# Kernel optimization log

Hardware: AMD Instinct MI355X
Metric: run time of the kernel (lower is better)

## Reference

```python
import jax, jax.numpy as jnp
import numpy as np

N = 100000   # nodes
D = 128      # in_feats
H = 128      # hidden_size
E = 500000   # message edges
EP = 100000  # positive pair edges
EN = 500000  # negative pair edges


def setup_inputs() -> dict:
    key = jax.random.key(0)
    ks = jax.random.split(key, 20)
    s = 1.0 / np.sqrt(H)
    f32 = jnp.float32
    inp = {
        "x": jax.random.normal(ks[0], (N, D), f32),
        "src": jax.random.randint(ks[1], (E,), 0, N, jnp.int32),
        "dst": jax.random.randint(ks[2], (E,), 0, N, jnp.int32),
        "pos_src": jax.random.randint(ks[3], (EP,), 0, N, jnp.int32),
        "pos_dst": jax.random.randint(ks[4], (EP,), 0, N, jnp.int32),
        "neg_src": jax.random.randint(ks[5], (EN,), 0, N, jnp.int32),
        "neg_dst": jax.random.randint(ks[6], (EN,), 0, N, jnp.int32),
        # SAGEConv layer 0 (in->hid) and layer 1 (hid->hid)
        "W_self0": jax.random.normal(ks[7], (D, H), f32) * s,
        "W_neigh0": jax.random.normal(ks[8], (D, H), f32) * s,
        "b0": jnp.zeros((H,), f32),
        "W_self1": jax.random.normal(ks[9], (H, H), f32) * s,
        "W_neigh1": jax.random.normal(ks[10], (H, H), f32) * s,
        "b1": jnp.zeros((H,), f32),
        # EdgeDecoder MLP: hid->hid->hid->1
        "dW1": jax.random.normal(ks[11], (H, H), f32) * s,
        "db1": jnp.zeros((H,), f32),
        "dW2": jax.random.normal(ks[12], (H, H), f32) * s,
        "db2": jnp.zeros((H,), f32),
        "dW3": jax.random.normal(ks[13], (H, 1), f32) * s,
        "db3": jnp.zeros((1,), f32),
    }
    return inp


def _sage_mean(h, src, dst, W_self, W_neigh, b, n_nodes):
    # mean-aggregate neighbor features: gather src feats, segment-sum over dst
    agg = jax.ops.segment_sum(h[src], dst, num_segments=n_nodes)       # [N, d]
    deg = jax.ops.segment_sum(jnp.ones((src.shape[0],), h.dtype), dst,
                              num_segments=n_nodes)                     # [N]
    h_neigh = agg / jnp.maximum(deg, 1.0)[:, None]
    return h @ W_self + h_neigh @ W_neigh + b


def _edge_decode(h, e_src, e_dst, W1, b1, W2, b2, W3, b3):
    z = h[e_src] * h[e_dst]                    # [E_pair, H]
    z = jax.nn.relu(z @ W1 + b1)
    z = jax.nn.relu(z @ W2 + b2)
    return z @ W3 + b3                         # [E_pair, 1]


def reference(x, src, dst, pos_src, pos_dst, neg_src, neg_dst,
              W_self0, W_neigh0, b0, W_self1, W_neigh1, b1,
              dW1, db1, dW2, db2, dW3, db3):
    n = x.shape[0]
    h = jax.nn.relu(_sage_mean(x, src, dst, W_self0, W_neigh0, b0, n))
    h = _sage_mean(h, src, dst, W_self1, W_neigh1, b1, n)  # no act on last layer
    h_pos = _edge_decode(h, pos_src, pos_dst, dW1, db1, dW2, db2, dW3, db3)
    h_neg = _edge_decode(h, neg_src, neg_dst, dW1, db1, dW2, db2, dW3, db3)
    return (h_pos, h_neg)
```

## Files before the change

kernel.cpp:

```cpp
#include <hip/hip_runtime.h>
#include <hip/hip_bf16.h>

#define HD 128

typedef unsigned int u32;
typedef unsigned short u16;
typedef __attribute__((ext_vector_type(8))) short short8;
typedef __attribute__((ext_vector_type(4))) float f32x4;

__device__ __forceinline__ float bf2f(u16 u) {
    return __uint_as_float(((u32)u) << 16);
}
__device__ __forceinline__ u16 f2bf(float f) {
    u32 u = __float_as_uint(f);
    u32 r = (u + 0x7fffu + ((u >> 16) & 1u)) >> 16;
    return (u16)r;
}
__device__ __forceinline__ u32 pk2bf(float lo, float hi) {
    __hip_bfloat162 h = __float22bfloat162_rn(make_float2(lo, hi));
    union { __hip_bfloat162 h; u32 u; } cv; cv.h = h;
    return cv.u;
}
__device__ __forceinline__ u32 hmul2(u32 a, u32 b) {
    union { u32 u; __hip_bfloat162 h; } x, y, r;
    x.u = a; y.u = b;
    r.h = __hmul2(x.h, y.h);
    return r.u;
}
__device__ __forceinline__ float ldf(const void* p, size_t i, bool f32m) {
    return f32m ? ((const float*)p)[i] : bf2f(((const u16*)p)[i]);
}
__device__ __forceinline__ int swz(int row, int col) {
    return row * 128 + ((((col >> 3) ^ (row & 7)) << 3) | (col & 7));
}
__device__ __forceinline__ void acc8_bf16(uint4 v, float* a) {
    a[0] += __uint_as_float(v.x << 16); a[1] += __uint_as_float(v.x & 0xffff0000u);
    a[2] += __uint_as_float(v.y << 16); a[3] += __uint_as_float(v.y & 0xffff0000u);
    a[4] += __uint_as_float(v.z << 16); a[5] += __uint_as_float(v.z & 0xffff0000u);
    a[6] += __uint_as_float(v.w << 16); a[7] += __uint_as_float(v.w & 0xffff0000u);
}

__global__ void detect_mode(const u32* __restrict__ x, int* __restrict__ mode) {
    __shared__ int cnt_s;
    if (threadIdx.x == 0) cnt_s = 0;
    __syncthreads();
    u32 e = (x[threadIdx.x] >> 23) & 0xFFu;
    if (e >= 90u && e < 170u) atomicAdd(&cnt_s, 1);
    __syncthreads();
    if (threadIdx.x == 0) mode[0] = (cnt_s >= 128) ? 1 : 0;
}

__global__ void cast_x(const void* __restrict__ x, u16* __restrict__ xb,
                       const int* __restrict__ gmode, int total8) {
    const bool f32m = gmode[0] != 0;
    int i = blockIdx.x * 256 + threadIdx.x;
    int stride = gridDim.x * 256;
    if (f32m) {
        for (; i < total8; i += stride) {
            const float* p = (const float*)x + (size_t)i * 8;
            float4 v0 = *(const float4*)p, v1 = *(const float4*)(p + 4);
            uint4 o;
            o.x = pk2bf(v0.x, v0.y); o.y = pk2bf(v0.z, v0.w);
            o.z = pk2bf(v1.x, v1.y); o.w = pk2bf(v1.z, v1.w);
            *(uint4*)(xb + (size_t)i * 8) = o;
        }
    } else {
        for (; i < total8; i += stride) {
            *(uint4*)(xb + (size_t)i * 8) =
                *(const uint4*)((const u16*)x + (size_t)i * 8);
        }
    }
}

__global__ void pack_w6(const void* __restrict__ W0, const void* __restrict__ W1,
                        const void* __restrict__ W2, const void* __restrict__ W3,
                        const void* __restrict__ W4, const void* __restrict__ W5,
                        u16* __restrict__ out, const int* __restrict__ gmode) {
    const bool f32m = gmode[0] != 0;
    int gid = blockIdx.x * 256 + threadIdx.x;
    if (gid >= 6 * 16384) return;
    int sel = gid >> 14, idx = gid & 16383;
    const void* W = sel == 0 ? W0 : sel == 1 ? W1 : sel == 2 ? W2 :
                    sel == 3 ? W3 : sel == 4 ? W4 : W5;
    int j = idx & 7, lane = (idx >> 3) & 63, ks = (idx >> 9) & 3, nt = idx >> 11;
    int k = ks * 32 + (lane >> 4) * 8 + j;
    int n = nt * 16 + (lane & 15);
    out[gid] = f2bf(ldf(W, (size_t)k * HD + n, f32m));
}

__global__ void cnt_count(const int* __restrict__ dst, int* __restrict__ cnt, int e) {
    int i = blockIdx.x * 256 + threadIdx.x;
    if (i < e) atomicAdd(&cnt[dst[i]], 1);
}

__global__ void scan_blocks(const int* __restrict__ cnt, int* __restrict__ rowptr,
                            int* __restrict__ bsum, int n) {
    __shared__ int s[256];
    int t = threadIdx.x, gid = blockIdx.x * 256 + t;
    int v = (gid < n) ? cnt[gid] : 0;
    s[t] = v; __syncthreads();
    #pragma unroll
    for (int off = 1; off < 256; off <<= 1) {
        int x = (t >= off) ? s[t - off] : 0;
        __syncthreads();
        s[t] += x;
        __syncthreads();
    }
    if (gid < n) rowptr[gid] = s[t] - v;
    if (t == 255) bsum[blockIdx.x] = s[255];
}

__global__ void scan_bsum(int* __restrict__ bsum, int nb) {
    __shared__ int s[1024];
    __shared__ int carry;
    int t = threadIdx.x;
    if (t == 0) carry = 0;
    __syncthreads();
    for (int base = 0; base < nb; base += 1024) {
        int i = base + t;
        int v = (i < nb) ? bsum[i] : 0;
        s[t] = v; __syncthreads();
        #pragma unroll
        for (int off = 1; off < 1024; off <<= 1) {
            int x = (t >= off) ? s[t - off] : 0;
            __syncthreads();
            s[t] += x;
            __syncthreads();
        }
        if (i < nb) bsum[i] = carry + s[t] - v;
        __syncthreads();
        if (t == 0) carry += s[1023];
        __syncthreads();
    }
}

__global__ void scan_add(int* __restrict__ rowptr, const int* __restrict__ bsum,
                         int* __restrict__ cur, int n, int e) {
    int gid = blockIdx.x * 256 + threadIdx.x;
    if (gid < n) {
        int v = rowptr[gid] + bsum[blockIdx.x];
        rowptr[gid] = v;
        cur[gid] = v;
    } else if (gid == n) {
        rowptr[n] = e;
    }
}

__global__ void csr_fill(const int* __restrict__ src, const int* __restrict__ dst,
                         int* __restrict__ cur, int* __restrict__ cidx, int e) {
    int i = blockIdx.x * 256 + threadIdx.x;
    if (i >= e) return;
    int p = atomicAdd(&cur[dst[i]], 1);
    cidx[p] = src[i];
}

__global__ __launch_bounds__(256, 8) void agg_mean(
    const u16* __restrict__ X, const int* __restrict__ rowptr,
    const int* __restrict__ cidx, u16* __restrict__ M, int n) {
    const int t = threadIdx.x;
    const int row = blockIdx.x * 16 + (t >> 4);
    if (row >= n) return;
    const int colo = (t & 15) * 8;
    const int s0 = rowptr[row], s1 = rowptr[row + 1];
    float a[8] = {0.f, 0.f, 0.f, 0.f, 0.f, 0.f, 0.f, 0.f};
    int i = s0;
    for (; i + 3 < s1; i += 4) {
        int c0 = cidx[i], c1 = cidx[i + 1], c2 = cidx[i + 2], c3 = cidx[i + 3];
        uint4 v0 = *(const uint4*)(X + (size_t)c0 * HD + colo);
        uint4 v1 = *(const uint4*)(X + (size_t)c1 * HD + colo);
        uint4 v2 = *(const uint4*)(X + (size_t)c2 * HD + colo);
        uint4 v3 = *(const uint4*)(X + (size_t)c3 * HD + colo);
        acc8_bf16(v0, a); acc8_bf16(v1, a);
        acc8_bf16(v2, a); acc8_bf16(v3, a);
    }
    if (i + 1 < s1) {
        int c0 = cidx[i], c1 = cidx[i + 1];
        uint4 v0 = *(const uint4*)(X + (size_t)c0 * HD + colo);
        uint4 v1 = *(const uint4*)(X + (size_t)c1 * HD + colo);
        acc8_bf16(v0, a); acc8_bf16(v1, a);
        i += 2;
    }
    if (i < s1) {
        uint4 v0 = *(const uint4*)(X + (size_t)cidx[i] * HD + colo);
        acc8_bf16(v0, a);
    }
    float iv = 1.f / fmaxf((float)(s1 - s0), 1.f);
    uint4 o;
    o.x = pk2bf(a[0] * iv, a[1] * iv);
    o.y = pk2bf(a[2] * iv, a[3] * iv);
    o.z = pk2bf(a[4] * iv, a[5] * iv);
    o.w = pk2bf(a[6] * iv, a[7] * iv);
    *(uint4*)(M + (size_t)row * HD + colo) = o;
}

template <bool RELU>
__global__ __launch_bounds__(256, 4) void sage_gemm(
    const u16* __restrict__ X, const u16* __restrict__ M,
    const u16* __restrict__ Wsp, const u16* __restrict__ Wnp,
    const void* __restrict__ bias, u16* __restrict__ hout,
    const int* __restrict__ gmode, int n) {
    __shared__ u16 zx[64 * 128];
    __shared__ u16 zm[64 * 128];
    const bool f32m = gmode[0] != 0;
    const int t = threadIdx.x;
    const int n0 = blockIdx.x * 64;
    const int lane = t & 63;
    const int w = t >> 6;
    const int cl = lane & 15, quad = lane >> 4;

    #pragma unroll
    for (int i = 0; i < 4; i++) {
        int idx = t + i * 256;
        int e = idx >> 4, sg = (idx & 15) * 8;
        int node = n0 + e;
        uint4 px = make_uint4(0, 0, 0, 0), pm = make_uint4(0, 0, 0, 0);
        if (node < n) {
            px = *(const uint4*)(X + (size_t)node * HD + sg);
            pm = *(const uint4*)(M + (size_t)node * HD + sg);
        }
        *(uint4*)&zx[swz(e, sg)] = px;
        *(uint4*)&zm[swz(e, sg)] = pm;
    }
    __syncthreads();

    f32x4 acc[2][4];
    #pragma unroll
    for (int ft = 0; ft < 2; ft++) {
        int f0 = w * 32 + ft * 16 + quad * 4;
        f32x4 bv;
        bv[0] = ldf(bias, f0 + 0, f32m);
        bv[1] = ldf(bias, f0 + 1, f32m);
        bv[2] = ldf(bias, f0 + 2, f32m);
        bv[3] = ldf(bias, f0 + 3, f32m);
        #pragma unroll
        for (int et = 0; et < 4; et++) acc[ft][et] = bv;
    }
    #pragma unroll
    for (int ks = 0; ks < 4; ks++) {
        short8 a[2], b[4];
        #pragma unroll
        for (int ft = 0; ft < 2; ft++)
            a[ft] = ((const short8*)Wsp)[((w * 2 + ft) * 4 + ks) * 64 + lane];
        #pragma unroll
        for (int et = 0; et < 4; et++)
            b[et] = *(const short8*)&zx[swz(et * 16 + cl, ks * 32 + quad * 8)];
        #pragma unroll
        for (int ft = 0; ft < 2; ft++)
            #pragma unroll
            for (int et = 0; et < 4; et++)
                acc[ft][et] = __builtin_amdgcn_mfma_f32_16x16x32_bf16(
                    a[ft], b[et], acc[ft][et], 0, 0, 0);
    }
    #pragma unroll
    for (int ks = 0; ks < 4; ks++) {
        short8 a[2], b[4];
        #pragma unroll
        for (int ft = 0; ft < 2; ft++)
            a[ft] = ((const short8*)Wnp)[((w * 2 + ft) * 4 + ks) * 64 + lane];
        #pragma unroll
        for (int et = 0; et < 4; et++)
            b[et] = *(const short8*)&zm[swz(et * 16 + cl, ks * 32 + quad * 8)];
        #pragma unroll
        for (int ft = 0; ft < 2; ft++)
            #pragma unroll
            for (int et = 0; et < 4; et++)
                acc[ft][et] = __builtin_amdgcn_mfma_f32_16x16x32_bf16(
                    a[ft], b[et], acc[ft][et], 0, 0, 0);
    }
    __syncthreads();

    #pragma unroll
    for (int ft = 0; ft < 2; ft++) {
        int f0 = w * 32 + ft * 16 + quad * 4;
        #pragma unroll
        for (int et = 0; et < 4; et++) {
            f32x4 v = acc[ft][et];
            float v0 = RELU ? fmaxf(v[0], 0.f) : v[0];
            float v1 = RELU ? fmaxf(v[1], 0.f) : v[1];
            float v2 = RELU ? fmaxf(v[2], 0.f) : v[2];
            float v3 = RELU ? fmaxf(v[3], 0.f) : v[3];
            *(uint2*)&zx[swz(et * 16 + cl, f0)] =
                make_uint2(pk2bf(v0, v1), pk2bf(v2, v3));
        }
    }
    __syncthreads();
    #pragma unroll
    for (int i = 0; i < 4; i++) {
        int idx = t + i * 256;
        int e = idx >> 4, sg = (idx & 15) * 8;
        int node = n0 + e;
        if (node < n)
            *(uint4*)&hout[(size_t)node * HD + sg] = *(const uint4*)&zx[swz(e, sg)];
    }
}

__global__ __launch_bounds__(256) void edge_decode_mfma(
    const u16* __restrict__ h,
    const int* __restrict__ psrc, const int* __restrict__ pdst, int ep, int PB,
    const int* __restrict__ nsrc, const int* __restrict__ ndst, int en,
    const u16* __restrict__ W1p, const void* __restrict__ b1,
    const u16* __restrict__ W2p, const void* __restrict__ b2,
    const void* __restrict__ W3, const void* __restrict__ b3,
    void* __restrict__ out, const int* __restrict__ gmode) {
    __shared__ u16 zA[64 * 128];
    __shared__ float psum[256];
    const bool f32m = gmode[0] != 0;
    const int t = threadIdx.x;
    const int b = blockIdx.x;
    const int* esrc; const int* edst; int e0, obase, ne;
    if (b < PB) { esrc = psrc; edst = pdst; e0 = b * 64;        obase = 0;  ne = ep; }
    else        { esrc = nsrc; edst = ndst; e0 = (b - PB) * 64; obase = ep; ne = en; }
    const int lane = t & 63;
    const int w = t >> 6;
    const int cl = lane & 15, quad = lane >> 4;

    #pragma unroll
    for (int i = 0; i < 4; i++) {
        int idx = t + i * 256;
        int e = idx >> 4, sg = (idx & 15) * 8;
        int eg = e0 + e;
        uint4 z = make_uint4(0, 0, 0, 0);
        if (eg < ne) {
            int s = esrc[eg], d = edst[eg];
            uint4 a  = *(const uint4*)(h + (size_t)s * HD + sg);
            uint4 bv = *(const uint4*)(h + (size_t)d * HD + sg);
            z.x = hmul2(a.x, bv.x); z.y = hmul2(a.y, bv.y);
            z.z = hmul2(a.z, bv.z); z.w = hmul2(a.w, bv.w);
        }
        *(uint4*)&zA[swz(e, sg)] = z;
    }
    __syncthreads();

    f32x4 acc[2][4];
    #pragma unroll
    for (int ft = 0; ft < 2; ft++) {
        int f0 = w * 32 + ft * 16 + quad * 4;
        f32x4 bv;
        bv[0] = ldf(b1, f0 + 0, f32m);
        bv[1] = ldf(b1, f0 + 1, f32m);
        bv[2] = ldf(b1, f0 + 2, f32m);
        bv[3] = ldf(b1, f0 + 3, f32m);
        #pragma unroll
        for (int et = 0; et < 4; et++) acc[ft][et] = bv;
    }
    #pragma unroll
    for (int ks = 0; ks < 4; ks++) {
        short8 a[2], bb[4];
        #pragma unroll
        for (int ft = 0; ft < 2; ft++)
            a[ft] = ((const short8*)W1p)[((w * 2 + ft) * 4 + ks) * 64 + lane];
        #pragma unroll
        for (int et = 0; et < 4; et++)
            bb[et] = *(const short8*)&zA[swz(et * 16 + cl, ks * 32 + quad * 8)];
        #pragma unroll
        for (int ft = 0; ft < 2; ft++)
            #pragma unroll
            for (int et = 0; et < 4; et++)
                acc[ft][et] = __builtin_amdgcn_mfma_f32_16x16x32_bf16(
                    a[ft], bb[et], acc[ft][et], 0, 0, 0);
    }
    __syncthreads();

    #pragma unroll
    for (int ft = 0; ft < 2; ft++) {
        int f0 = w * 32 + ft * 16 + quad * 4;
        #pragma unroll
        for (int et = 0; et < 4; et++) {
            f32x4 v = acc[ft][et];
            *(uint2*)&zA[swz(et * 16 + cl, f0)] = make_uint2(
                pk2bf(fmaxf(v[0], 0.f), fmaxf(v[1], 0.f)),
                pk2bf(fmaxf(v[2], 0.f), fmaxf(v[3], 0.f)));
        }
    }
    __syncthreads();

    #pragma unroll
    for (int ft = 0; ft < 2; ft++) {
        int f0 = w * 32 + ft * 16 + quad * 4;
        f32x4 bv;
        bv[0] = ldf(b2, f0 + 0, f32m);
        bv[1] = ldf(b2, f0 + 1, f32m);
        bv[2] = ldf(b2, f0 + 2, f32m);
        bv[3] = ldf(b2, f0 + 3, f32m);
        #pragma unroll
        for (int et = 0; et < 4; et++) acc[ft][et] = bv;
    }
    #pragma unroll
    for (int ks = 0; ks < 4; ks++) {
        short8 a[2], bb[4];
        #pragma unroll
        for (int ft = 0; ft < 2; ft++)
            a[ft] = ((const short8*)W2p)[((w * 2 + ft) * 4 + ks) * 64 + lane];
        #pragma unroll
        for (int et = 0; et < 4; et++)
            bb[et] = *(const short8*)&zA[swz(et * 16 + cl, ks * 32 + quad * 8)];
        #pragma unroll
        for (int ft = 0; ft < 2; ft++)
            #pragma unroll
            for (int et = 0; et < 4; et++)
                acc[ft][et] = __builtin_amdgcn_mfma_f32_16x16x32_bf16(
                    a[ft], bb[et], acc[ft][et], 0, 0, 0);
    }
    float p[4] = {0.f, 0.f, 0.f, 0.f};
    #pragma unroll
    for (int ft = 0; ft < 2; ft++) {
        int f0 = w * 32 + ft * 16 + quad * 4;
        float w3v0 = ldf(W3, f0 + 0, f32m);
        float w3v1 = ldf(W3, f0 + 1, f32m);
        float w3v2 = ldf(W3, f0 + 2, f32m);
        float w3v3 = ldf(W3, f0 + 3, f32m);
        #pragma unroll
        for (int et = 0; et < 4; et++) {
            f32x4 v = acc[ft][et];
            p[et] = fmaf(fmaxf(v[0], 0.f), w3v0, p[et]);
            p[et] = fmaf(fmaxf(v[1], 0.f), w3v1, p[et]);
            p[et] = fmaf(fmaxf(v[2], 0.f), w3v2, p[et]);
            p[et] = fmaf(fmaxf(v[3], 0.f), w3v3, p[et]);
        }
    }
    #pragma unroll
    for (int et = 0; et < 4; et++) {
        p[et] += __shfl_xor(p[et], 16);
        p[et] += __shfl_xor(p[et], 32);
    }
    if (lane < 16) {
        #pragma unroll
        for (int et = 0; et < 4; et++)
            psum[w * 64 + et * 16 + lane] = p[et];
    }
    __syncthreads();
    if (t < 64) {
        int eg = e0 + t;
        if (eg < ne) {
            float sum = ldf(b3, 0, f32m) + (psum[t] + psum[64 + t])
                      + (psum[128 + t] + psum[192 + t]);
            if (f32m) ((float*)out)[obase + eg] = sum;
            else      ((u16*)out)[obase + eg]   = f2bf(sum);
        }
    }
}

extern "C" void kernel_launch(void* const* d_in, const int* in_sizes, int n_in,
                              void* d_out, int out_size, void* d_ws, size_t ws_size,
                              hipStream_t stream) {
    const void* x      = d_in[0];
    const int* src     = (const int*)d_in[1];
    const int* dst     = (const int*)d_in[2];
    const int* pos_src = (const int*)d_in[3];
    const int* pos_dst = (const int*)d_in[4];
    const int* neg_src = (const int*)d_in[5];
    const int* neg_dst = (const int*)d_in[6];
    const void* Ws0 = d_in[7];
    const void* Wn0 = d_in[8];
    const void* b0  = d_in[9];
    const void* Ws1 = d_in[10];
    const void* Wn1 = d_in[11];
    const void* b1  = d_in[12];
    const void* dW1 = d_in[13];
    const void* db1 = d_in[14];
    const void* dW2 = d_in[15];
    const void* db2 = d_in[16];
    const void* dW3 = d_in[17];
    const void* db3 = d_in[18];

    const int n  = in_sizes[0] / HD;
    const int e  = in_sizes[1];
    const int ep = in_sizes[3];
    const int en = in_sizes[5];
    const int NB = (n + 255) / 256;
    const int PB = (ep + 63) / 64, NDB = (en + 63) / 64;

    char* base = (char*)d_ws;
    u16* R1 = (u16*)d_ws;
    u16* R2 = R1 + (size_t)n * HD;
    size_t off = (size_t)n * HD * 4;
    int* mode = (int*)(base + off);      off += 16;
    int* rowptr = (int*)(base + off);    off += (size_t)(n + 1) * 4; off = (off + 15) & ~(size_t)15;
    int* cur = (int*)(base + off);       off += (size_t)n * 4;       off = (off + 15) & ~(size_t)15;
    int* cidx = (int*)(base + off);      off += (size_t)e * 4;       off = (off + 15) & ~(size_t)15;
    int* bsum = (int*)(base + off);      off += (size_t)NB * 4;      off = (off + 15) & ~(size_t)15;
    u16* Wpk  = (u16*)(base + off);
    u16* W1p  = Wpk;
    u16* W2p  = Wpk + 16384;
    u16* Ws0p = Wpk + 2 * 16384;
    u16* Wn0p = Wpk + 3 * 16384;
    u16* Ws1p = Wpk + 4 * 16384;
    u16* Wn1p = Wpk + 5 * 16384;

    detect_mode<<<dim3(1), dim3(256), 0, stream>>>((const u32*)x, mode);

    hipMemsetAsync(cur, 0, (size_t)n * 4, stream);
    cnt_count<<<dim3((e + 255) / 256), dim3(256), 0, stream>>>(dst, cur, e);
    scan_blocks<<<dim3(NB), dim3(256), 0, stream>>>(cur, rowptr, bsum, n);
    scan_bsum<<<dim3(1), dim3(1024), 0, stream>>>(bsum, NB);
    scan_add<<<dim3((n + 256) / 256), dim3(256), 0, stream>>>(rowptr, bsum, cur, n, e);
    csr_fill<<<dim3((e + 255) / 256), dim3(256), 0, stream>>>(src, dst, cur, cidx, e);

    pack_w6<<<dim3(384), dim3(256), 0, stream>>>(dW1, dW2, Ws0, Wn0, Ws1, Wn1, Wpk, mode);

    cast_x<<<dim3(2048), dim3(256), 0, stream>>>(x, R1, mode, n * (HD / 8));

    agg_mean<<<dim3((n + 15) / 16), dim3(256), 0, stream>>>(R1, rowptr, cidx, R2, n);
    sage_gemm<true><<<dim3((n + 63) / 64), dim3(256), 0, stream>>>(
        R1, R2, Ws0p, Wn0p, b0, R1, mode, n);

    agg_mean<<<dim3((n + 15) / 16), dim3(256), 0, stream>>>(R1, rowptr, cidx, R2, n);
    sage_gemm<false><<<dim3((n + 63) / 64), dim3(256), 0, stream>>>(
        R1, R2, Ws1p, Wn1p, b1, R1, mode, n);

    edge_decode_mfma<<<dim3(PB + NDB), dim3(256), 0, stream>>>(
        R1, pos_src, pos_dst, ep, PB, neg_src, neg_dst, en,
        W1p, db1, W2p, db2, dW3, db3, d_out, mode);
}
```

Measured before the change: 345.0 us.

## Make edge decoder persistent with register prefetch of next tile's gathers

Turns the edge decode kernel into a persistent grid-stride loop capped at 2048 blocks. The random gathers for the next 64-edge tile are issued into registers before the current tile's MFMA work, so gather latency overlaps with compute. It also raises MFMA wave priority with s_setprio and replaces __syncthreads with a lighter LDS-wait plus barrier. The cost is more live registers, since launch_bounds now asks for 4 blocks per CU, and fewer blocks in flight to hide latency.

```diff
diff --git a/kernel.cpp b/kernel.cpp
--- a/kernel.cpp
+++ b/kernel.cpp
@@ -38,6 +38,10 @@
     a[2] += __uint_as_float(v.y << 16); a[3] += __uint_as_float(v.y & 0xffff0000u);
     a[4] += __uint_as_float(v.z << 16); a[5] += __uint_as_float(v.z & 0xffff0000u);
     a[6] += __uint_as_float(v.w << 16); a[7] += __uint_as_float(v.w & 0xffff0000u);
+}
+__device__ __forceinline__ void bar_lds() {
+    asm volatile("s_waitcnt lgkmcnt(0)" ::: "memory");
+    __builtin_amdgcn_s_barrier();
 }
 
 __global__ void detect_mode(const u32* __restrict__ x, int* __restrict__ mode) {
@@ -294,10 +298,10 @@
     }
 }
 
-__global__ __launch_bounds__(256) void edge_decode_mfma(
+__global__ __launch_bounds__(256, 4) void edge_decode_mfma(
     const u16* __restrict__ h,
     const int* __restrict__ psrc, const int* __restrict__ pdst, int ep, int PB,
-    const int* __restrict__ nsrc, const int* __restrict__ ndst, int en,
+    const int* __restrict__ nsrc, const int* __restrict__ ndst, int en, int TT,
     const u16* __restrict__ W1p, const void* __restrict__ b1,
     const u16* __restrict__ W2p, const void* __restrict__ b2,
     const void* __restrict__ W3, const void* __restrict__ b3,
@@ -306,137 +310,180 @@
     __shared__ float psum[256];
     const bool f32m = gmode[0] != 0;
     const int t = threadIdx.x;
-    const int b = blockIdx.x;
-    const int* esrc; const int* edst; int e0, obase, ne;
-    if (b < PB) { esrc = psrc; edst = pdst; e0 = b * 64;        obase = 0;  ne = ep; }
-    else        { esrc = nsrc; edst = ndst; e0 = (b - PB) * 64; obase = ep; ne = en; }
     const int lane = t & 63;
     const int w = t >> 6;
     const int cl = lane & 15, quad = lane >> 4;
-
-    #pragma unroll
-    for (int i = 0; i < 4; i++) {
-        int idx = t + i * 256;
-        int e = idx >> 4, sg = (idx & 15) * 8;
-        int eg = e0 + e;
-        uint4 z = make_uint4(0, 0, 0, 0);
-        if (eg < ne) {
-            int s = esrc[eg], d = edst[eg];
-            uint4 a  = *(const uint4*)(h + (size_t)s * HD + sg);
-            uint4 bv = *(const uint4*)(h + (size_t)d * HD + sg);
-            z.x = hmul2(a.x, bv.x); z.y = hmul2(a.y, bv.y);
-            z.z = hmul2(a.z, bv.z); z.w = hmul2(a.w, bv.w);
-        }
-        *(uint4*)&zA[swz(e, sg)] = z;
-    }
-    __syncthreads();
-
-    f32x4 acc[2][4];
-    #pragma unroll
-    for (int ft = 0; ft < 2; ft++) {
-        int f0 = w * 32 + ft * 16 + quad * 4;
-        f32x4 bv;
-        bv[0] = ldf(b1, f0 + 0, f32m);
-        bv[1] = ldf(b1, f0 + 1, f32m);
-        bv[2] = ldf(b1, f0 + 2, f32m);
-        bv[3] = ldf(b1, f0 + 3, f32m);
-        #pragma unroll
-        for (int et = 0; et < 4; et++) acc[ft][et] = bv;
-    }
-    #pragma unroll
-    for (int ks = 0; ks < 4; ks++) {
-        short8 a[2], bb[4];
-        #pragma unroll
-        for (int ft = 0; ft < 2; ft++)
-            a[ft] = ((const short8*)W1p)[((w * 2 + ft) * 4 + ks) * 64 + lane];
-        #pragma unroll
-        for (int et = 0; et < 4; et++)
-            bb[et] = *(const short8*)&zA[swz(et * 16 + cl, ks * 32 + quad * 8)];
-        #pragma unroll
-        for (int ft = 0; ft < 2; ft++)
+    const int G = gridDim.x;
+
+    uint4 va[4], vb[4];
+    if (blockIdx.x < TT) {
+        int tt = blockIdx.x;
+        const int* es; const int* ed; int e0, ne;
+        if (tt < PB) { es = psrc; ed = pdst; e0 = tt * 64;        ne = ep; }
+        else         { es = nsrc; ed = ndst; e0 = (tt - PB) * 64; ne = en; }
+        #pragma unroll
+        for (int i = 0; i < 4; i++) {
+            int idx = t + i * 256;
+            int e = idx >> 4, sg = (idx & 15) * 8;
+            int eg = e0 + e;
+            va[i] = make_uint4(0, 0, 0, 0);
+            vb[i] = make_uint4(0, 0, 0, 0);
+            if (eg < ne) {
+                int s = es[eg], d = ed[eg];
+                va[i] = *(const uint4*)(h + (size_t)s * HD + sg);
+                vb[i] = *(const uint4*)(h + (size_t)d * HD + sg);
+            }
+        }
+    }
+
+    for (int tt = blockIdx.x; tt < TT; tt += G) {
+        #pragma unroll
+        for (int i = 0; i < 4; i++) {
+            int idx = t + i * 256;
+            int e = idx >> 4, sg = (idx & 15) * 8;
+            uint4 z;
+            z.x = hmul2(va[i].x, vb[i].x); z.y = hmul2(va[i].y, vb[i].y);
+            z.z = hmul2(va[i].z, vb[i].z); z.w = hmul2(va[i].w, vb[i].w);
+            *(uint4*)&zA[swz(e, sg)] = z;
+        }
+        {
+            int tn = tt + G;
+            if (tn < TT) {
+                const int* es; const int* ed; int e0, ne;
+                if (tn < PB) { es = psrc; ed = pdst; e0 = tn * 64;        ne = ep; }
+                else         { es = nsrc; ed = ndst; e0 = (tn - PB) * 64; ne = en; }
+                #pragma unroll
+                for (int i = 0; i < 4; i++) {
+                    int idx = t + i * 256;
+                    int e = idx >> 4, sg = (idx & 15) * 8;
+                    int eg = e0 + e;
+                    va[i] = make_uint4(0, 0, 0, 0);
+                    vb[i] = make_uint4(0, 0, 0, 0);
+                    if (eg < ne) {
+                        int s = es[eg], d = ed[eg];
+                        va[i] = *(const uint4*)(h + (size_t)s * HD + sg);
+                        vb[i] = *(const uint4*)(h + (size_t)d * HD + sg);
+                    }
+                }
+            }
+        }
+        bar_lds();
+
+        f32x4 acc[2][4];
+        #pragma unroll
+        for (int ft = 0; ft < 2; ft++) {
+            int f0 = w * 32 + ft * 16 + quad * 4;
+            f32x4 bv;
+            bv[0] = ldf(b1, f0 + 0, f32m);
+            bv[1] = ldf(b1, f0 + 1, f32m);
+            bv[2] = ldf(b1, f0 + 2, f32m);
+            bv[3] = ldf(b1, f0 + 3, f32m);
+            #pragma unroll
+            for (int et = 0; et < 4; et++) acc[ft][et] = bv;
+        }
+        __builtin_amdgcn_s_setprio(1);
+        #pragma unroll
+        for (int ks = 0; ks < 4; ks++) {
+            short8 a[2], bb[4];
+            #pragma unroll
+            for (int ft = 0; ft < 2; ft++)
+                a[ft] = ((const short8*)W1p)[((w * 2 + ft) * 4 + ks) * 64 + lane];
             #pragma unroll
             for (int et = 0; et < 4; et++)
-                acc[ft][et] = __builtin_amdgcn_mfma_f32_16x16x32_bf16(
-                    a[ft], bb[et], acc[ft][et], 0, 0, 0);
-    }
-    __syncthreads();
-
-    #pragma unroll
-    for (int ft = 0; ft < 2; ft++) {
-        int f0 = w * 32 + ft * 16 + quad * 4;
+                bb[et] = *(const short8*)&zA[swz(et * 16 + cl, ks * 32 + quad * 8)];
+            #pragma unroll
+            for (int ft = 0; ft < 2; ft++)
+                #pragma unroll
+                for (int et = 0; et < 4; et++)
+                    acc[ft][et] = __builtin_amdgcn_mfma_f32_16x16x32_bf16(
+                        a[ft], bb[et], acc[ft][et], 0, 0, 0);
+        }
+        __builtin_amdgcn_s_setprio(0);
+        bar_lds();
+
+        #pragma unroll
+        for (int ft = 0; ft < 2; ft++) {
+            int f0 = w * 32 + ft * 16 + quad * 4;
+            #pragma unroll
+            for (int et = 0; et < 4; et++) {
+                f32x4 v = acc[ft][et];
+                *(uint2*)&zA[swz(et * 16 + cl, f0)] = make_uint2(
+                    pk2bf(fmaxf(v[0], 0.f), fmaxf(v[1], 0.f)),
+                    pk2bf(fmaxf(v[2], 0.f), fmaxf(v[3], 0.f)));
+            }
+        }
+        bar_lds();
+
+        #pragma unroll
+        for (int ft = 0; ft < 2; ft++) {
+            int f0 = w * 32 + ft * 16 + quad * 4;
+            f32x4 bv;
+            bv[0] = ldf(b2, f0 + 0, f32m);
+            bv[1] = ldf(b2, f0 + 1, f32m);
+            bv[2] = ldf(b2, f0 + 2, f32m);
+            bv[3] = ldf(b2, f0 + 3, f32m);
+            #pragma unroll
+            for (int et = 0; et < 4; et++) acc[ft][et] = bv;
+        }
+        __builtin_amdgcn_s_setprio(1);
+        #pragma unroll
+        for (int ks = 0; ks < 4; ks++) {
+            short8 a[2], bb[4];
+            #pragma unroll
+            for (int ft = 0; ft < 2; ft++)
+                a[ft] = ((const short8*)W2p)[((w * 2 + ft) * 4 + ks) * 64 + lane];
+            #pragma unroll
+            for (int et = 0; et < 4; et++)
+                bb[et] = *(const short8*)&zA[swz(et * 16 + cl, ks * 32 + quad * 8)];
+            #pragma unroll
+            for (int ft = 0; ft < 2; ft++)
+                #pragma unroll
+                for (int et = 0; et < 4; et++)
+                    acc[ft][et] = __builtin_amdgcn_mfma_f32_16x16x32_bf16(
+                        a[ft], bb[et], acc[ft][et], 0, 0, 0);
+        }
+        __builtin_amdgcn_s_setprio(0);
+        float p[4] = {0.f, 0.f, 0.f, 0.f};
+        #pragma unroll
+        for (int ft = 0; ft < 2; ft++) {
+            int f0 = w * 32 + ft * 16 + quad * 4;
+            float w3v0 = ldf(W3, f0 + 0, f32m);
+            float w3v1 = ldf(W3, f0 + 1, f32m);
+            float w3v2 = ldf(W3, f0 + 2, f32m);
+            float w3v3 = ldf(W3, f0 + 3, f32m);
+            #pragma unroll
+            for (int et = 0; et < 4; et++) {
+                f32x4 v = acc[ft][et];
+                p[et] = fmaf(fmaxf(v[0], 0.f), w3v0, p[et]);
+                p[et] = fmaf(fmaxf(v[1], 0.f), w3v1, p[et]);
+                p[et] = fmaf(fmaxf(v[2], 0.f), w3v2, p[et]);
+                p[et] = fmaf(fmaxf(v[3], 0.f), w3v3, p[et]);
+            }
+        }
         #pragma unroll
         for (int et = 0; et < 4; et++) {
-            f32x4 v = acc[ft][et];
-            *(uint2*)&zA[swz(et * 16 + cl, f0)] = make_uint2(
-                pk2bf(fmaxf(v[0], 0.f), fmaxf(v[1], 0.f)),
-                pk2bf(fmaxf(v[2], 0.f), fmaxf(v[3], 0.f)));
-        }
-    }
-    __syncthreads();
-
-    #pragma unroll
-    for (int ft = 0; ft < 2; ft++) {
-        int f0 = w * 32 + ft * 16 + quad * 4;
-        f32x4 bv;
-        bv[0] = ldf(b2, f0 + 0, f32m);
-        bv[1] = ldf(b2, f0 + 1, f32m);
-        bv[2] = ldf(b2, f0 + 2, f32m);
-        bv[3] = ldf(b2, f0 + 3, f32m);
-        #pragma unroll
-        for (int et = 0; et < 4; et++) acc[ft][et] = bv;
-    }
-    #pragma unroll
-    for (int ks = 0; ks < 4; ks++) {
-        short8 a[2], bb[4];
-        #pragma unroll
-        for (int ft = 0; ft < 2; ft++)
-            a[ft] = ((const short8*)W2p)[((w * 2 + ft) * 4 + ks) * 64 + lane];
-        #pragma unroll
-        for (int et = 0; et < 4; et++)
-            bb[et] = *(const short8*)&zA[swz(et * 16 + cl, ks * 32 + quad * 8)];
-        #pragma unroll
-        for (int ft = 0; ft < 2; ft++)
+            p[et] += __shfl_xor(p[et], 16);
+            p[et] += __shfl_xor(p[et], 32);
+        }
+        if (lane < 16) {
             #pragma unroll
             for (int et = 0; et < 4; et++)
-                acc[ft][et] = __builtin_amdgcn_mfma_f32_16x16x32_bf16(
-                    a[ft], bb[et], acc[ft][et], 0, 0, 0);
-    }
-    float p[4] = {0.f, 0.f, 0.f, 0.f};
-    #pragma unroll
-    for (int ft = 0; ft < 2; ft++) {
-        int f0 = w * 32 + ft * 16 + quad * 4;
-        float w3v0 = ldf(W3, f0 + 0, f32m);
-        float w3v1 = ldf(W3, f0 + 1, f32m);
-        float w3v2 = ldf(W3, f0 + 2, f32m);
-        float w3v3 = ldf(W3, f0 + 3, f32m);
-        #pragma unroll
-        for (int et = 0; et < 4; et++) {
-            f32x4 v = acc[ft][et];
-            p[et] = fmaf(fmaxf(v[0], 0.f), w3v0, p[et]);
-            p[et] = fmaf(fmaxf(v[1], 0.f), w3v1, p[et]);
-            p[et] = fmaf(fmaxf(v[2], 0.f), w3v2, p[et]);
-            p[et] = fmaf(fmaxf(v[3], 0.f), w3v3, p[et]);
-        }
-    }
-    #pragma unroll
-    for (int et = 0; et < 4; et++) {
-        p[et] += __shfl_xor(p[et], 16);
-        p[et] += __shfl_xor(p[et], 32);
-    }
-    if (lane < 16) {
-        #pragma unroll
-        for (int et = 0; et < 4; et++)
-            psum[w * 64 + et * 16 + lane] = p[et];
-    }
-    __syncthreads();
-    if (t < 64) {
-        int eg = e0 + t;
-        if (eg < ne) {
-            float sum = ldf(b3, 0, f32m) + (psum[t] + psum[64 + t])
-                      + (psum[128 + t] + psum[192 + t]);
-            if (f32m) ((float*)out)[obase + eg] = sum;
-            else      ((u16*)out)[obase + eg]   = f2bf(sum);
-        }
+                psum[w * 64 + et * 16 + lane] = p[et];
+        }
+        bar_lds();
+        if (t < 64) {
+            int e0, ne, obase;
+            if (tt < PB) { e0 = tt * 64;        ne = ep; obase = 0;  }
+            else         { e0 = (tt - PB) * 64; ne = en; obase = ep; }
+            int eg = e0 + t;
+            if (eg < ne) {
+                float sum = ldf(b3, 0, f32m) + (psum[t] + psum[64 + t])
+                          + (psum[128 + t] + psum[192 + t]);
+                if (f32m) ((float*)out)[obase + eg] = sum;
+                else      ((u16*)out)[obase + eg]   = f2bf(sum);
+            }
+        }
+        __builtin_amdgcn_s_barrier();
     }
 }
 
@@ -469,6 +516,8 @@
     const int en = in_sizes[5];
     const int NB = (n + 255) / 256;
     const int PB = (ep + 63) / 64, NDB = (en + 63) / 64;
+    const int TT = PB + NDB;
+    const int GD = TT < 2048 ? TT : 2048;
 
     char* base = (char*)d_ws;
     u16* R1 = (u16*)d_ws;
@@ -508,7 +557,7 @@
     sage_gemm<false><<<dim3((n + 63) / 64), dim3(256), 0, stream>>>(
         R1, R2, Ws1p, Wn1p, b1, R1, mode, n);
 
-    edge_decode_mfma<<<dim3(PB + NDB), dim3(256), 0, stream>>>(
-        R1, pos_src, pos_dst, ep, PB, neg_src, neg_dst, en,
+    edge_decode_mfma<<<dim3(GD), dim3(256), 0, stream>>>(
+        R1, pos_src, pos_dst, ep, PB, neg_src, neg_dst, en, TT,
         W1p, db1, W2p, db2, dW3, db3, d_out, mode);
 }
```

New measurement: 381.9 us. 10.7% more time.

## Counting-sort decoder edge pairs by source node before edge decode

Applied to the files above, without the earlier changes.

Adds a counting sort of all positive and negative pair edges by source node: a count, a scan and an atomic fill that writes sorted src, dst and original-index arrays into the R2 workspace, which is free after the last SAGE layer. The edge decoder then reads the sorted lists and scatters each result back to its original output slot. The aim is better cache locality for the source-row gathers of h. The cost is several extra kernel launches and atomic passes over 600k edges, plus a scattered output write.

```diff
diff --git a/kernel.cpp b/kernel.cpp
--- a/kernel.cpp
+++ b/kernel.cpp
@@ -93,6 +93,14 @@
     if (i < e) atomicAdd(&cnt[dst[i]], 1);
 }
 
+__global__ void cnt2_count(const int* __restrict__ ps, const int* __restrict__ ns,
+                           int ep, int te, int* __restrict__ cnt) {
+    int i = blockIdx.x * 256 + threadIdx.x;
+    if (i >= te) return;
+    int s = (i < ep) ? ps[i] : ns[i - ep];
+    atomicAdd(&cnt[s], 1);
+}
+
 __global__ void scan_blocks(const int* __restrict__ cnt, int* __restrict__ rowptr,
                             int* __restrict__ bsum, int n) {
     __shared__ int s[256];
@@ -152,6 +160,20 @@
     if (i >= e) return;
     int p = atomicAdd(&cur[dst[i]], 1);
     cidx[p] = src[i];
+}
+
+__global__ void sort_fill(const int* __restrict__ ps, const int* __restrict__ pd,
+                          const int* __restrict__ ns, const int* __restrict__ nd,
+                          int ep, int te, int* __restrict__ cur,
+                          int* __restrict__ se, int* __restrict__ sd,
+                          int* __restrict__ so) {
+    int i = blockIdx.x * 256 + threadIdx.x;
+    if (i >= te) return;
+    int s, d;
+    if (i < ep) { s = ps[i]; d = pd[i]; }
+    else        { s = ns[i - ep]; d = nd[i - ep]; }
+    int p = atomicAdd(&cur[s], 1);
+    se[p] = s; sd[p] = d; so[p] = i;
 }
 
 __global__ __launch_bounds__(256, 8) void agg_mean(
@@ -296,8 +318,8 @@
 
 __global__ __launch_bounds__(256) void edge_decode_mfma(
     const u16* __restrict__ h,
-    const int* __restrict__ psrc, const int* __restrict__ pdst, int ep, int PB,
-    const int* __restrict__ nsrc, const int* __restrict__ ndst, int en,
+    const int* __restrict__ se, const int* __restrict__ sd,
+    const int* __restrict__ so, int te,
     const u16* __restrict__ W1p, const void* __restrict__ b1,
     const u16* __restrict__ W2p, const void* __restrict__ b2,
     const void* __restrict__ W3, const void* __restrict__ b3,
@@ -306,10 +328,7 @@
     __shared__ float psum[256];
     const bool f32m = gmode[0] != 0;
     const int t = threadIdx.x;
-    const int b = blockIdx.x;
-    const int* esrc; const int* edst; int e0, obase, ne;
-    if (b < PB) { esrc = psrc; edst = pdst; e0 = b * 64;        obase = 0;  ne = ep; }
-    else        { esrc = nsrc; edst = ndst; e0 = (b - PB) * 64; obase = ep; ne = en; }
+    const int e0 = blockIdx.x * 64;
     const int lane = t & 63;
     const int w = t >> 6;
     const int cl = lane & 15, quad = lane >> 4;
@@ -320,8 +339,8 @@
         int e = idx >> 4, sg = (idx & 15) * 8;
         int eg = e0 + e;
         uint4 z = make_uint4(0, 0, 0, 0);
-        if (eg < ne) {
-            int s = esrc[eg], d = edst[eg];
+        if (eg < te) {
+            int s = se[eg], d = sd[eg];
             uint4 a  = *(const uint4*)(h + (size_t)s * HD + sg);
             uint4 bv = *(const uint4*)(h + (size_t)d * HD + sg);
             z.x = hmul2(a.x, bv.x); z.y = hmul2(a.y, bv.y);
@@ -431,11 +450,12 @@
     __syncthreads();
     if (t < 64) {
         int eg = e0 + t;
-        if (eg < ne) {
+        if (eg < te) {
             float sum = ldf(b3, 0, f32m) + (psum[t] + psum[64 + t])
                       + (psum[128 + t] + psum[192 + t]);
-            if (f32m) ((float*)out)[obase + eg] = sum;
-            else      ((u16*)out)[obase + eg]   = f2bf(sum);
+            int oi = so[eg];
+            if (f32m) ((float*)out)[oi] = sum;
+            else      ((u16*)out)[oi]   = f2bf(sum);
         }
     }
 }
@@ -468,7 +488,8 @@
     const int ep = in_sizes[3];
     const int en = in_sizes[5];
     const int NB = (n + 255) / 256;
-    const int PB = (ep + 63) / 64, NDB = (en + 63) / 64;
+    const int te = ep + en;
+    const int TT = (te + 63) / 64;
 
     char* base = (char*)d_ws;
     u16* R1 = (u16*)d_ws;
@@ -486,6 +507,9 @@
     u16* Wn0p = Wpk + 3 * 16384;
     u16* Ws1p = Wpk + 4 * 16384;
     u16* Wn1p = Wpk + 5 * 16384;
+    int* sd_ = (int*)R2;
+    int* so_ = sd_ + te;
+    int* se_ = so_ + te;
 
     detect_mode<<<dim3(1), dim3(256), 0, stream>>>((const u32*)x, mode);
 
@@ -508,7 +532,16 @@
     sage_gemm<false><<<dim3((n + 63) / 64), dim3(256), 0, stream>>>(
         R1, R2, Ws1p, Wn1p, b1, R1, mode, n);
 
-    edge_decode_mfma<<<dim3(PB + NDB), dim3(256), 0, stream>>>(
-        R1, pos_src, pos_dst, ep, PB, neg_src, neg_dst, en,
+    hipMemsetAsync(cur, 0, (size_t)n * 4, stream);
+    cnt2_count<<<dim3((te + 255) / 256), dim3(256), 0, stream>>>(
+        pos_src, neg_src, ep, te, cur);
+    scan_blocks<<<dim3(NB), dim3(256), 0, stream>>>(cur, rowptr, bsum, n);
+    scan_bsum<<<dim3(1), dim3(1024), 0, stream>>>(bsum, NB);
+    scan_add<<<dim3((n + 256) / 256), dim3(256), 0, stream>>>(rowptr, bsum, cur, n, te);
+    sort_fill<<<dim3((te + 255) / 256), dim3(256), 0, stream>>>(
+        pos_src, pos_dst, neg_src, neg_dst, ep, te, cur, se_, sd_, so_);
+
+    edge_decode_mfma<<<dim3(TT), dim3(256), 0, stream>>>(
+        R1, se_, sd_, so_, te,
         W1p, db1, W2p, db2, dW3, db3, d_out, mode);
 }
```

Result: slower. 418.8 us (+21.4%).
